# Optimization experiments

Hardware: AMD Instinct MI355X
Metric: run time of the kernel (lower is better)

## Reference

```python
import jax, jax.numpy as jnp
import numpy as np

BETA = 0.25  # init kwarg; exercises the 0 <= beta < 1 loss branch


def setup_inputs() -> dict:
    key = jax.random.key(0)
    k1, k2 = jax.random.split(key)
    N, D, K = 65536, 64, 4096
    x = jax.random.normal(k1, (N, D), dtype=jnp.float32)
    # original: uniform(-1/K, 1/K) then mean-centered; exact init distribution
    codebook = jax.random.uniform(k2, (K, D), dtype=jnp.float32,
                                  minval=-1.0 / K, maxval=1.0 / K)
    codebook = codebook - codebook.mean(axis=0, keepdims=True)
    return {"x": x, "codebook": codebook}


def reference(x, codebook):
    # pairwise squared distances via sum-of-squares + matmul: [N, K]
    dist = (jnp.sum(x * x, axis=1, keepdims=True)
            + jnp.sum(codebook * codebook, axis=1)
            - 2.0 * jnp.matmul(x, codebook.T))
    encoding_inds = jnp.argmin(dist, axis=1)            # [N]
    # gather codebook rows (equivalent to one-hot @ codebook, no one-hot materialized)
    quantized = jnp.take(codebook, encoding_inds, axis=0)  # [N, D]
    # straight-through estimator
    x_quantized = x + jax.lax.stop_gradient(quantized - x)
    mse = lambda a, b: jnp.mean((a - b) ** 2)
    loss = (BETA * mse(x, jax.lax.stop_gradient(quantized))
            + mse(quantized, jax.lax.stop_gradient(x)))
    return x_quantized, encoding_inds[:, None], loss
```

## Files before the change

### kernel.cpp

```cpp
#include <hip/hip_runtime.h>


#define D  64
#define NT 256

typedef unsigned short u16;
typedef short bf16x8 __attribute__((ext_vector_type(8)));
typedef float f32x4  __attribute__((ext_vector_type(4)));

#define VMWAIT(n) asm volatile("s_waitcnt vmcnt(" #n ")" ::: "memory")

__device__ __forceinline__ u16 f32_to_bf16_raw(float f) {
    union { float f; unsigned u; } v; v.f = f;
    unsigned u = v.u;
    u += 0x7FFFu + ((u >> 16) & 1u);
    return (u16)(u >> 16);
}
__device__ __forceinline__ float bf16_raw_to_f32(u16 h) {
    union { unsigned u; float f; } v; v.u = ((unsigned)h) << 16;
    return v.f;
}
__device__ __forceinline__ f32x4 mfma16(bf16x8 a, bf16x8 b, f32x4 c) {
    return __builtin_amdgcn_mfma_f32_16x16x32_bf16(a, b, c, 0, 0, 0);
}

__device__ __forceinline__ float np_pairwise_sumsq_64(const float* p) {
    float r[8];
    #pragma unroll
    for (int j = 0; j < 8; ++j) r[j] = __fmul_rn(p[j], p[j]);
    #pragma unroll
    for (int i = 8; i < 64; i += 8) {
        #pragma unroll
        for (int j = 0; j < 8; ++j)
            r[j] = __fadd_rn(r[j], __fmul_rn(p[i + j], p[i + j]));
    }
    float t0 = __fadd_rn(r[0], r[1]);
    float t1 = __fadd_rn(r[2], r[3]);
    float t2 = __fadd_rn(r[4], r[5]);
    float t3 = __fadd_rn(r[6], r[7]);
    return __fadd_rn(__fadd_rn(t0, t1), __fadd_rn(t2, t3));
}

__global__ __launch_bounds__(256) void prep_kernel(const float* __restrict__ x,
                                                   const float* __restrict__ cb,
                                                   float* __restrict__ sx,
                                                   float* __restrict__ sc,
                                                   bf16x8* __restrict__ cbf,
                                                   int* __restrict__ amb_cnt) {
    int b = blockIdx.x;
    if (b == 0 && threadIdx.x == 0) *amb_cnt = 0;
    if (b < 272) {
        const float* a = (b < 256) ? x : cb;
        float* o = (b < 256) ? sx : sc;
        int r0 = (b < 256) ? b * 256 : (b - 256) * 256;
        int r = r0 + threadIdx.x;
        float buf[64];
        const float4* p = (const float4*)(a + (size_t)r * D);
        #pragma unroll
        for (int i = 0; i < 16; ++i) {
            float4 v = p[i];
            buf[4*i] = v.x; buf[4*i+1] = v.y; buf[4*i+2] = v.z; buf[4*i+3] = v.w;
        }
        o[r] = np_pairwise_sumsq_64(buf);
    } else {
        int t = b - 272;
        int tid = threadIdx.x;
        int lane = tid & 63;
        int ks = (tid >> 6) & 1;
        int hl = tid >> 7;
        int code = t * 16 + (lane & 15);
        int g = lane >> 4;
        bf16x8 v;
        #pragma unroll
        for (int j = 0; j < 8; ++j) {
            int d = ks * 32 + g * 4 + (j & 3) + 16 * (j >> 2);
            float val = cb[(size_t)code * D + d];
            u16 h = f32_to_bf16_raw(val);
            if (hl) {
                float resid = val - bf16_raw_to_f32(h);
                h = f32_to_bf16_raw(resid);
            }
            v[j] = (short)h;
        }
        cbf[((size_t)t * 4 + hl * 2 + ks) * 64 + lane] = v;
    }
}

#define MARG_A 8.0e-6f
#define MARG_B 5.0e-7f

__global__ __launch_bounds__(256, 2) void phase1_kernel(
    const float* __restrict__ x, const float* __restrict__ sx,
    const float* __restrict__ sc, const bf16x8* __restrict__ cbf,
    int* __restrict__ idxbuf, int* __restrict__ amb_cnt, int* __restrict__ amb_rows)
{
    __shared__ __align__(16) char ring[4][3][4096];
    __shared__ float scl[4096];
    __shared__ float lm1[128][2], lm2[128][2];
    __shared__ int   li1[128][2];

    const int tid  = threadIdx.x;
    const int w    = tid >> 6;
    const int lane = tid & 63;
    const int r = lane & 15, g = lane >> 4;
    const int half = w & 1;
    const int rowg = w >> 1;
    const int wbase = blockIdx.x * 128 + rowg * 64;

    for (int j = tid; j < 1024; j += 256)
        *(float4*)&scl[j * 4] = *(const float4*)&sc[j * 4];
    __syncthreads();

    bf16x8 Ah0[4], Ah1[4], Al0[4], Al1[4];
    #pragma unroll
    for (int s = 0; s < 4; ++s) {
        const float* xr = x + (size_t)(wbase + s * 16 + r) * D;
        float e0[8], e1[8];
        float4 f0 = *(const float4*)(xr + g * 4);
        float4 f1 = *(const float4*)(xr + 16 + g * 4);
        float4 f2 = *(const float4*)(xr + 32 + g * 4);
        float4 f3 = *(const float4*)(xr + 48 + g * 4);
        e0[0]=f0.x;e0[1]=f0.y;e0[2]=f0.z;e0[3]=f0.w; e0[4]=f1.x;e0[5]=f1.y;e0[6]=f1.z;e0[7]=f1.w;
        e1[0]=f2.x;e1[1]=f2.y;e1[2]=f2.z;e1[3]=f2.w; e1[4]=f3.x;e1[5]=f3.y;e1[6]=f3.z;e1[7]=f3.w;
        #pragma unroll
        for (int j = 0; j < 8; ++j) {
            u16 h0 = f32_to_bf16_raw(e0[j]);
            Ah0[s][j] = (short)h0;
            Al0[s][j] = (short)f32_to_bf16_raw(e0[j] - bf16_raw_to_f32(h0));
            u16 h1 = f32_to_bf16_raw(e1[j]);
            Ah1[s][j] = (short)h1;
            Al1[s][j] = (short)f32_to_bf16_raw(e1[j] - bf16_raw_to_f32(h1));
        }
    }

    float sxr[16], m1[16], m2[16];
    int   i1[16];
    #pragma unroll
    for (int u = 0; u < 16; ++u) {
        sxr[u] = sx[wbase + (u >> 2) * 16 + g * 4 + (u & 3)];
        m1[u] = 3.4e38f; m2[u] = 3.4e38f; i1[u] = 0;
    }

    const int t0 = half * 128;
    char* ringbase = &ring[w][0][0];

    auto stage = [&](int t, int buf) {
        const char* src = (const char*)cbf + (size_t)t * 4096 + lane * 16;
        char* dst = ringbase + buf * 4096 + lane * 16;
        #pragma unroll
        for (int i = 0; i < 4; ++i)
            __builtin_amdgcn_global_load_lds(
                (const __attribute__((address_space(1))) unsigned int*)(src + i * 1024),
                (__attribute__((address_space(3))) unsigned int*)(dst + i * 1024),
                16, 0, 0);
    };

    auto compute = [&](int t, int buf) {
        const bf16x8* bfr = (const bf16x8*)(ringbase + buf * 4096);
        bf16x8 b0h = bfr[0 * 64 + lane];
        bf16x8 b1h = bfr[1 * 64 + lane];
        bf16x8 b0l = bfr[2 * 64 + lane];
        bf16x8 b1l = bfr[3 * 64 + lane];
        float sck = scl[t * 16 + r];
        int   kc  = t * 16 + r;

        f32x4 acc[4];
        __builtin_amdgcn_s_setprio(1);
        #pragma unroll
        for (int s = 0; s < 4; ++s) {
            f32x4 a = {0.f, 0.f, 0.f, 0.f};
            a = mfma16(Ah0[s], b0h, a);
            a = mfma16(Ah1[s], b1h, a);
            a = mfma16(Ah0[s], b0l, a);
            a = mfma16(Ah1[s], b1l, a);
            a = mfma16(Al0[s], b0h, a);
            a = mfma16(Al1[s], b1h, a);
            acc[s] = a;
        }
        __builtin_amdgcn_s_setprio(0);

        #pragma unroll
        for (int s = 0; s < 4; ++s) {
            #pragma unroll
            for (int q = 0; q < 4; ++q) {
                int u = s * 4 + q;
                float sv = __fmaf_rn(-2.0f, acc[s][q], __fadd_rn(sxr[u], sck));
                m2[u] = fminf(m2[u], fmaxf(m1[u], sv));
                bool lt = sv < m1[u];
                i1[u] = lt ? kc : i1[u];
                m1[u] = fminf(m1[u], sv);
            }
        }
    };

    VMWAIT(0);
    stage(t0 + 0, 0); stage(t0 + 1, 1); stage(t0 + 2, 2);

    #pragma unroll 1
    for (int i = 0; i < 125; ++i) {
        VMWAIT(8);
        compute(t0 + i, i % 3);
        asm volatile("s_waitcnt lgkmcnt(0)" ::: "memory");
        __builtin_amdgcn_sched_barrier(0);
        stage(t0 + i + 3, i % 3);
    }
    VMWAIT(8); compute(t0 + 125, 125 % 3);
    VMWAIT(4); compute(t0 + 126, 126 % 3);
    VMWAIT(0); compute(t0 + 127, 127 % 3);

    #pragma unroll
    for (int u = 0; u < 16; ++u) {
        #pragma unroll
        for (int mm = 1; mm < 16; mm <<= 1) {
            float om1 = __shfl_xor(m1[u], mm, 64);
            float om2 = __shfl_xor(m2[u], mm, 64);
            int   oi1 = __shfl_xor(i1[u], mm, 64);
            float nm2 = fminf(fmaxf(m1[u], om1), fminf(m2[u], om2));
            i1[u] = (om1 < m1[u]) ? oi1 : i1[u];
            m1[u] = fminf(m1[u], om1);
            m2[u] = nm2;
        }
    }
    if (r == 0) {
        #pragma unroll
        for (int u = 0; u < 16; ++u) {
            int rowin = rowg * 64 + (u >> 2) * 16 + g * 4 + (u & 3);
            lm1[rowin][half] = m1[u];
            lm2[rowin][half] = m2[u];
            li1[rowin][half] = i1[u];
        }
    }
    __syncthreads();

    if (tid < 128) {
        float a1 = lm1[tid][0], b1 = lm1[tid][1];
        float a2 = lm2[tid][0], b2 = lm2[tid][1];
        int   ia = li1[tid][0], ib = li1[tid][1];
        float m1f = fminf(a1, b1);
        float m2f = fminf(fmaxf(a1, b1), fminf(a2, b2));
        int   i1f = (b1 < a1) ? ib : ia;
        int orow = blockIdx.x * 128 + tid;
        idxbuf[orow] = i1f;
        float marg = __fmaf_rn(sx[orow], MARG_B, MARG_A);
        if (m2f - m1f <= marg) {
            int slot = atomicAdd(amb_cnt, 1);
            amb_rows[slot] = orow;
        }
    }
}

__global__ __launch_bounds__(256) void exact_scan(
    const float* __restrict__ x, const float* __restrict__ cb,
    const float* __restrict__ sx, const float* __restrict__ sc,
    const int* __restrict__ amb_cnt, const int* __restrict__ amb_rows,
    int* __restrict__ idxbuf)
{
    __shared__ float csT[4][64][64];
    __shared__ float xsT[64][16];
    __shared__ float redv[16][64];
    __shared__ int   redi[16][64];
    __shared__ float sxl[16];
    __shared__ int   rowids[16];

    const int tid = threadIdx.x;
    const int cnt = *amb_cnt;
    const int tz = tid >> 6, ty = (tid >> 4) & 3, cx = tid & 15;

    for (int base = blockIdx.x * 16; base < cnt; base += gridDim.x * 16) {
        if (tid < 16) {
            int i = base + tid;
            int rr = (i < cnt) ? amb_rows[i] : amb_rows[base];
            rowids[tid] = rr;
            sxl[tid] = sx[rr];
        }
        __syncthreads();
        {
            int rr = rowids[tid >> 4];
            int dg = tid & 15;
            float4 v = *(const float4*)(x + (size_t)rr * D + dg * 4);
            xsT[dg*4+0][tid>>4] = v.x; xsT[dg*4+1][tid>>4] = v.y;
            xsT[dg*4+2][tid>>4] = v.z; xsT[dg*4+3][tid>>4] = v.w;
        }

        float bv[4]; int bi[4];
        #pragma unroll
        for (int i = 0; i < 4; ++i) { bv[i] = 3.4e38f; bi[i] = 0x7fffffff; }

        for (int st = 0; st < 16; ++st) {
            __syncthreads();
            {
                int code = st * 256 + tid;
                const float4* src = (const float4*)(cb + (size_t)code * D);
                #pragma unroll
                for (int dd = 0; dd < 16; ++dd) {
                    float4 v = src[dd];
                    csT[tid>>6][dd*4+0][tid&63] = v.x; csT[tid>>6][dd*4+1][tid&63] = v.y;
                    csT[tid>>6][dd*4+2][tid&63] = v.z; csT[tid>>6][dd*4+3][tid&63] = v.w;
                }
            }
            __syncthreads();

            float acc[4][4];
            #pragma unroll
            for (int i = 0; i < 4; ++i)
                #pragma unroll
                for (int j = 0; j < 4; ++j) acc[i][j] = 0.0f;

            #pragma unroll 4
            for (int d = 0; d < 64; ++d) {
                float4 xv = *(const float4*)&xsT[d][ty * 4];
                float4 cv = *(const float4*)&csT[tz][d][cx * 4];
                float xr[4] = {xv.x, xv.y, xv.z, xv.w};
                float cc[4] = {cv.x, cv.y, cv.z, cv.w};
                #pragma unroll
                for (int i = 0; i < 4; ++i)
                    #pragma unroll
                    for (int j = 0; j < 4; ++j)
                        acc[i][j] = __fmaf_rn(xr[i], cc[j], acc[i][j]);
            }
            #pragma unroll
            for (int j = 0; j < 4; ++j) {
                int k = st * 256 + tz * 64 + cx * 4 + j;
                float sck = sc[k];
                #pragma unroll
                for (int i = 0; i < 4; ++i) {
                    float tt = __fadd_rn(sxl[ty * 4 + i], sck);
                    float u  = __fmul_rn(2.0f, acc[i][j]);
                    float s  = __fsub_rn(tt, u);
                    if (s < bv[i] || (s == bv[i] && k < bi[i])) { bv[i] = s; bi[i] = k; }
                }
            }
        }

        #pragma unroll
        for (int i = 0; i < 4; ++i) { redv[ty*4+i][tz*16+cx] = bv[i]; redi[ty*4+i][tz*16+cx] = bi[i]; }
        __syncthreads();
        if (tid < 16) {
            float bvv = redv[tid][0]; int bii = redi[tid][0];
            #pragma unroll 8
            for (int i = 1; i < 64; ++i) {
                float v = redv[tid][i]; int k = redi[tid][i];
                if (v < bvv || (v == bvv && k < bii)) { bvv = v; bii = k; }
            }
            idxbuf[rowids[tid]] = bii;
        }
        __syncthreads();
    }
}

__global__ __launch_bounds__(256) void finalize_rows(
    const float* __restrict__ x, const float* __restrict__ cb,
    const int* __restrict__ idxbuf,
    float* __restrict__ out_q, float* __restrict__ out_i,
    double* __restrict__ partials, int N)
{
    __shared__ double wsum[4];
    int wid = threadIdx.x >> 6, lane = threadIdx.x & 63;
    int n = blockIdx.x * 4 + wid;

    int idx = idxbuf[n];
    float q  = cb[(size_t)idx * D + lane];
    float xv = x[(size_t)n * D + lane];
    out_q[(size_t)n * D + lane] = q;

    double diff = (double)xv - (double)q;
    double s = diff * diff;
    #pragma unroll
    for (int off = 32; off > 0; off >>= 1) s += __shfl_down(s, off, 64);
    if (lane == 0) { wsum[wid] = s; out_i[n] = (float)idx; }
    __syncthreads();
    if (threadIdx.x == 0) partials[blockIdx.x] = (wsum[0] + wsum[1]) + (wsum[2] + wsum[3]);
}

__global__ __launch_bounds__(256) void loss_kernel(const double* __restrict__ partials,
                                                   int nP, float* __restrict__ out_loss,
                                                   double invND)
{
    __shared__ double red[256];
    double s = 0.0;
    for (int i = threadIdx.x; i < nP; i += 256) s += partials[i];
    red[threadIdx.x] = s;
    __syncthreads();
    #pragma unroll
    for (int step = 128; step > 0; step >>= 1) {
        if ((int)threadIdx.x < step) red[threadIdx.x] += red[threadIdx.x + step];
        __syncthreads();
    }
    if (threadIdx.x == 0) {
        double m = red[0] * invND;
        out_loss[0] = (float)(0.25 * m + m);
    }
}

extern "C" void kernel_launch(void* const* d_in, const int* in_sizes, int n_in,
                              void* d_out, int out_size, void* d_ws, size_t ws_size,
                              hipStream_t stream)
{
    const float* x  = (const float*)d_in[0];
    const float* cb = (const float*)d_in[1];
    const int N = in_sizes[0] / D;
    const int K = in_sizes[1] / D;

    float* out      = (float*)d_out;
    float* out_q    = out;
    float* out_i    = out + (size_t)N * D;
    float* out_loss = out_i + N;

    char* ws = (char*)d_ws;
    bf16x8* cbf      = (bf16x8*)ws;
    size_t off = (size_t)(K / 16) * 4 * 64 * sizeof(bf16x8);
    float*  sx       = (float*)(ws + off);  off += (size_t)N * 4;
    float*  sc       = (float*)(ws + off);  off += (size_t)K * 4;
    int*    idxbuf   = (int*)(ws + off);    off += (size_t)N * 4;
    int*    amb_rows = (int*)(ws + off);    off += (size_t)N * 4;
    double* partials = (double*)(ws + off); off += (size_t)(N / 4) * 8;
    int*    amb_cnt  = (int*)(ws + off);

    prep_kernel<<<272 + K / 16, 256, 0, stream>>>(x, cb, sx, sc, cbf, amb_cnt);
    phase1_kernel<<<N / 128, 256, 0, stream>>>(x, sx, sc, cbf, idxbuf, amb_cnt, amb_rows);
    exact_scan<<<512, 256, 0, stream>>>(x, cb, sx, sc, amb_cnt, amb_rows, idxbuf);
    finalize_rows<<<N / 4, 256, 0, stream>>>(x, cb, idxbuf, out_q, out_i, partials, N);
    loss_kernel<<<1, 256, 0, stream>>>(partials, N / 4, out_loss,
                                       1.0 / ((double)N * (double)D));
}
```

Measured before the change: 265.3 us.

## Software-pipeline phase1 MFMA and VALU argmin across codebook tiles

Restructures the phase1 main loop so that each iteration issues the MFMA products for tile t+1 while doing the VALU min/argmin update for tile t. Three accumulator sets rotate through an unrolled-by-3 loop, and the LDS prefetch is issued alongside the LDS reads. The intent is to hide VALU epilogue latency behind matrix work and drop the per-iteration lgkmcnt wait and sched barrier, at the cost of more live registers. It also doubles the exact_scan grid to 1024 blocks.

After: 244.3 us. 7.9% less time.

```diff
diff --git a/kernel.cpp b/kernel.cpp
--- a/kernel.cpp
+++ b/kernel.cpp
@@ -8,7 +8,8 @@
 typedef short bf16x8 __attribute__((ext_vector_type(8)));
 typedef float f32x4  __attribute__((ext_vector_type(4)));
 
-#define VMWAIT(n) asm volatile("s_waitcnt vmcnt(" #n ")" ::: "memory")
+#define VMWAIT_(n) asm volatile("s_waitcnt vmcnt(" #n ")" ::: "memory")
+#define VMWAIT(n) VMWAIT_(n)
 
 __device__ __forceinline__ u16 f32_to_bf16_raw(float f) {
     union { float f; unsigned u; } v; v.f = f;
@@ -89,6 +90,67 @@
 #define MARG_A 8.0e-6f
 #define MARG_B 5.0e-7f
 
+#define STAGE(T, BUF) do {                                                    \
+    const char* _src = (const char*)cbf + (size_t)(T) * 4096 + lane * 16;     \
+    char* _dst = ringbase + (BUF) * 4096 + lane * 16;                         \
+    __builtin_amdgcn_global_load_lds((const __attribute__((address_space(1))) unsigned int*)(_src),        (__attribute__((address_space(3))) unsigned int*)(_dst),        16, 0, 0); \
+    __builtin_amdgcn_global_load_lds((const __attribute__((address_space(1))) unsigned int*)(_src + 1024), (__attribute__((address_space(3))) unsigned int*)(_dst + 1024), 16, 0, 0); \
+    __builtin_amdgcn_global_load_lds((const __attribute__((address_space(1))) unsigned int*)(_src + 2048), (__attribute__((address_space(3))) unsigned int*)(_dst + 2048), 16, 0, 0); \
+    __builtin_amdgcn_global_load_lds((const __attribute__((address_space(1))) unsigned int*)(_src + 3072), (__attribute__((address_space(3))) unsigned int*)(_dst + 3072), 16, 0, 0); \
+} while (0)
+
+#define DSREAD(T, BUF, SCK) do {                                              \
+    const bf16x8* _bfr = (const bf16x8*)(ringbase + (BUF) * 4096);            \
+    Fb0h = _bfr[lane]; Fb1h = _bfr[64 + lane];                                \
+    Fb0l = _bfr[128 + lane]; Fb1l = _bfr[192 + lane];                         \
+    SCK = scl[(T) * 16 + r];                                                  \
+} while (0)
+
+#define MFMAC(P) do {                                                         \
+    _Pragma("unroll")                                                         \
+    for (int s = 0; s < 4; ++s) {                                             \
+        f32x4 _a = {0.f, 0.f, 0.f, 0.f};                                      \
+        _a = mfma16(Ah0[s], Fb0h, _a);                                        \
+        _a = mfma16(Ah1[s], Fb1h, _a);                                        \
+        _a = mfma16(Ah0[s], Fb0l, _a);                                        \
+        _a = mfma16(Ah1[s], Fb1l, _a);                                        \
+        _a = mfma16(Al0[s], Fb0h, _a);                                        \
+        _a = mfma16(Al1[s], Fb1h, _a);                                        \
+        P[s] = _a;                                                            \
+    }                                                                         \
+} while (0)
+
+#define VALUU(P, SCK, T) do {                                                 \
+    int _kc = (T) * 16 + r;                                                   \
+    _Pragma("unroll")                                                         \
+    for (int s = 0; s < 4; ++s) {                                             \
+        _Pragma("unroll")                                                     \
+        for (int q = 0; q < 4; ++q) {                                         \
+            int u = s * 4 + q;                                                \
+            float sv = __fmaf_rn(-2.0f, P[s][q], __fadd_rn(sxr[u], SCK));     \
+            m2[u] = fminf(m2[u], fmaxf(m1[u], sv));                           \
+            bool lt = sv < m1[u];                                             \
+            i1[u] = lt ? _kc : i1[u];                                         \
+            m1[u] = fminf(m1[u], sv);                                         \
+        }                                                                     \
+    }                                                                         \
+} while (0)
+
+#define ITF(I, BR, BS, PA, PB, SA, SB) do {                                   \
+    VMWAIT(4);                                                                \
+    DSREAD(t0 + (I) + 2, BR, SB);                                             \
+    STAGE(t0 + (I) + 4, BS);                                                  \
+    VALUU(PA, SA, t0 + (I));                                                  \
+    MFMAC(PB);                                                                \
+} while (0)
+#define ITN(I, BR, PA, PB, SA, SB, WN) do {                                   \
+    VMWAIT(WN);                                                               \
+    DSREAD(t0 + (I) + 2, BR, SB);                                             \
+    VALUU(PA, SA, t0 + (I));                                                  \
+    MFMAC(PB);                                                                \
+} while (0)
+#define ITV(I, PA, SA) do { VALUU(PA, SA, t0 + (I)); } while (0)
+
 __global__ __launch_bounds__(256, 2) void phase1_kernel(
     const float* __restrict__ x, const float* __restrict__ sx,
     const float* __restrict__ sc, const bf16x8* __restrict__ cbf,
@@ -144,69 +206,29 @@
     const int t0 = half * 128;
     char* ringbase = &ring[w][0][0];
 
-    auto stage = [&](int t, int buf) {
-        const char* src = (const char*)cbf + (size_t)t * 4096 + lane * 16;
-        char* dst = ringbase + buf * 4096 + lane * 16;
-        #pragma unroll
-        for (int i = 0; i < 4; ++i)
-            __builtin_amdgcn_global_load_lds(
-                (const __attribute__((address_space(1))) unsigned int*)(src + i * 1024),
-                (__attribute__((address_space(3))) unsigned int*)(dst + i * 1024),
-                16, 0, 0);
-    };
-
-    auto compute = [&](int t, int buf) {
-        const bf16x8* bfr = (const bf16x8*)(ringbase + buf * 4096);
-        bf16x8 b0h = bfr[0 * 64 + lane];
-        bf16x8 b1h = bfr[1 * 64 + lane];
-        bf16x8 b0l = bfr[2 * 64 + lane];
-        bf16x8 b1l = bfr[3 * 64 + lane];
-        float sck = scl[t * 16 + r];
-        int   kc  = t * 16 + r;
-
-        f32x4 acc[4];
-        __builtin_amdgcn_s_setprio(1);
-        #pragma unroll
-        for (int s = 0; s < 4; ++s) {
-            f32x4 a = {0.f, 0.f, 0.f, 0.f};
-            a = mfma16(Ah0[s], b0h, a);
-            a = mfma16(Ah1[s], b1h, a);
-            a = mfma16(Ah0[s], b0l, a);
-            a = mfma16(Ah1[s], b1l, a);
-            a = mfma16(Al0[s], b0h, a);
-            a = mfma16(Al1[s], b1h, a);
-            acc[s] = a;
-        }
-        __builtin_amdgcn_s_setprio(0);
-
-        #pragma unroll
-        for (int s = 0; s < 4; ++s) {
-            #pragma unroll
-            for (int q = 0; q < 4; ++q) {
-                int u = s * 4 + q;
-                float sv = __fmaf_rn(-2.0f, acc[s][q], __fadd_rn(sxr[u], sck));
-                m2[u] = fminf(m2[u], fmaxf(m1[u], sv));
-                bool lt = sv < m1[u];
-                i1[u] = lt ? kc : i1[u];
-                m1[u] = fminf(m1[u], sv);
-            }
-        }
-    };
+    bf16x8 Fb0h, Fb1h, Fb0l, Fb1l;
+    f32x4  P0[4], P1[4], P2[4];
+    float  sck0, sck1, sck2;
 
     VMWAIT(0);
-    stage(t0 + 0, 0); stage(t0 + 1, 1); stage(t0 + 2, 2);
+    STAGE(t0 + 0, 0); STAGE(t0 + 1, 1);
+    VMWAIT(4); DSREAD(t0 + 0, 0, sck0); STAGE(t0 + 2, 2); MFMAC(P0);
+    VMWAIT(4); DSREAD(t0 + 1, 1, sck1); STAGE(t0 + 3, 0); MFMAC(P1);
 
     #pragma unroll 1
-    for (int i = 0; i < 125; ++i) {
-        VMWAIT(8);
-        compute(t0 + i, i % 3);
-        asm volatile("s_waitcnt lgkmcnt(0)" ::: "memory");
-        __builtin_amdgcn_sched_barrier(0);
-        stage(t0 + i + 3, i % 3);
-    }
-    VMWAIT(8); compute(t0 + 125, 125 % 3);
-    VMWAIT(4); compute(t0 + 126, 126 % 3);
-    VMWAIT(0); compute(t0 + 127, 127 % 3);
+    for (int i = 0; i < 120; i += 3) {
+        ITF(i + 0, 2, 1, P0, P2, sck0, sck2);
+        ITF(i + 1, 0, 2, P1, P0, sck1, sck0);
+        ITF(i + 2, 1, 0, P2, P1, sck2, sck1);
+    }
+    ITF(120, 2, 1, P0, P2, sck0, sck2);
+    ITF(121, 0, 2, P1, P0, sck1, sck0);
+    ITF(122, 1, 0, P2, P1, sck2, sck1);
+    ITF(123, 2, 1, P0, P2, sck0, sck2);
+    ITN(124, 0, P1, P0, sck1, sck0, 4);
+    ITN(125, 1, P2, P1, sck2, sck1, 0);
+    ITV(126, P0, sck0);
+    ITV(127, P1, sck1);
 
     #pragma unroll
     for (int u = 0; u < 16; ++u) {
@@ -418,7 +440,7 @@
 
     prep_kernel<<<272 + K / 16, 256, 0, stream>>>(x, cb, sx, sc, cbf, amb_cnt);
     phase1_kernel<<<N / 128, 256, 0, stream>>>(x, sx, sc, cbf, idxbuf, amb_cnt, amb_rows);
-    exact_scan<<<512, 256, 0, stream>>>(x, cb, sx, sc, amb_cnt, amb_rows, idxbuf);
+    exact_scan<<<1024, 256, 0, stream>>>(x, cb, sx, sc, amb_cnt, amb_rows, idxbuf);
     finalize_rows<<<N / 4, 256, 0, stream>>>(x, cb, idxbuf, out_q, out_i, partials, N);
     loss_kernel<<<1, 256, 0, stream>>>(partials, N / 4, out_loss,
                                        1.0 / ((double)N * (double)D));
```
